# Performance work log

Measured on AMD Instinct MI355X. Metric: run time of the kernel, lower is better.

## Reference

```python
import jax, jax.numpy as jnp
import numpy as np

DIM, DEPTH, HEADS, DIM_HEAD, MLP = 1024, 4, 16, 64, 4096
INNER = HEADS * DIM_HEAD
B, N = 2, 1024


def _ln(x, g, b, eps=1e-5):
    mu = jnp.mean(x, axis=-1, keepdims=True)
    var = jnp.mean(jnp.square(x - mu), axis=-1, keepdims=True)
    return (x - mu) * jax.lax.rsqrt(var + eps) * g + b


def setup_inputs() -> dict:
    key = jax.random.key(0)
    ks = jax.random.split(key, 8)
    s = 0.02
    return {
        "x": jax.random.normal(ks[0], (B, N, DIM), jnp.float32),
        "mask": jax.random.randint(ks[1], (B, N, N), 0, 2, jnp.int32),
        "ln1_g": jnp.ones((DEPTH, DIM), jnp.float32),
        "ln1_b": jnp.zeros((DEPTH, DIM), jnp.float32),
        "qkv_w": jax.random.normal(ks[2], (DEPTH, DIM, 3 * INNER), jnp.float32) * s,
        "out_w": jax.random.normal(ks[3], (DEPTH, INNER, DIM), jnp.float32) * s,
        "out_b": jnp.zeros((DEPTH, DIM), jnp.float32),
        "ln2_g": jnp.ones((DEPTH, DIM), jnp.float32),
        "ln2_b": jnp.zeros((DEPTH, DIM), jnp.float32),
        "ff1_w": jax.random.normal(ks[4], (DEPTH, DIM, MLP), jnp.float32) * s,
        "ff1_b": jnp.zeros((DEPTH, MLP), jnp.float32),
        "ff2_w": jax.random.normal(ks[5], (DEPTH, MLP, DIM), jnp.float32) * s,
        "ff2_b": jnp.zeros((DEPTH, DIM), jnp.float32),
    }


def reference(x, mask, ln1_g, ln1_b, qkv_w, out_w, out_b, ln2_g, ln2_b,
              ff1_w, ff1_b, ff2_w, ff2_b):
    scale = DIM_HEAD ** -0.5
    masked = (mask == 0)[:, None, :, :]  # [B,1,N,N], True -> fill -1e9
    b, n, _ = x.shape
    for l in range(DEPTH):
        # --- prenorm attention ---
        h = _ln(x, ln1_g[l], ln1_b[l])
        qkv = h @ qkv_w[l]  # [B,N,3*INNER]
        q, k, v = jnp.split(qkv, 3, axis=-1)
        q = q.reshape(b, n, HEADS, DIM_HEAD).transpose(0, 2, 1, 3)
        k = k.reshape(b, n, HEADS, DIM_HEAD).transpose(0, 2, 1, 3)
        v = v.reshape(b, n, HEADS, DIM_HEAD).transpose(0, 2, 1, 3)
        dots = jnp.einsum('bhqd,bhkd->bhqk', q, k) * scale
        dots = jnp.where(masked, jnp.float32(-1e9), dots)
        attn = jax.nn.softmax(dots, axis=-1)
        o = jnp.einsum('bhqk,bhkd->bhqd', attn, v)
        o = o.transpose(0, 2, 1, 3).reshape(b, n, INNER)
        x = o @ out_w[l] + out_b[l] + x
        # --- prenorm feedforward ---
        h = _ln(x, ln2_g[l], ln2_b[l])
        h = jax.nn.gelu(h @ ff1_w[l] + ff1_b[l], approximate=False)
        x = h @ ff2_w[l] + ff2_b[l] + x
    return x
```

## Files before the change

kernel.cpp:

```cpp
#include <hip/hip_runtime.h>
#include <stdint.h>

#define DIMM 1024
#define NSEQ 1024
#define BB 2
#define HEADSN 16
#define MLPD 4096
#define DEPTHN 4
#define MROWS (BB*NSEQ)
#define VSTR 10240

typedef __bf16 bf16x8 __attribute__((ext_vector_type(8)));
typedef float f32x4 __attribute__((ext_vector_type(4)));

__device__ __forceinline__ float bf2f(unsigned short u) {
    union { uint32_t i; float f; } x; x.i = ((uint32_t)u) << 16; return x.f;
}
__device__ __forceinline__ unsigned short f2bf(float f) {
    union { uint32_t i; float f; } x; x.f = f;
    uint32_t r = x.i + 0x7fffu + ((x.i >> 16) & 1u);
    return (unsigned short)(r >> 16);
}
__device__ __forceinline__ float loadf(const void* p, size_t i, int f32) {
    return f32 ? ((const float*)p)[i] : bf2f(((const unsigned short*)p)[i]);
}
__device__ __forceinline__ uint32_t cvt_pk_bf16(float lo, float hi) {
    uint32_t r;
    asm("v_cvt_pk_bf16_f32 %0, %1, %2" : "=v"(r) : "v"(lo), "v"(hi));
    return r;
}

__device__ __forceinline__ void gl_lds16(const unsigned short* g, unsigned short* l) {
    __builtin_amdgcn_global_load_lds(
        (const __attribute__((address_space(1))) uint32_t*)g,
        (__attribute__((address_space(3))) uint32_t*)l,
        16, 0, 0);
}

__global__ __launch_bounds__(256) void sniff_kernel(const unsigned short* __restrict__ x,
                                                    int* __restrict__ flag) {
    __shared__ int cnt[256];
    int tid = threadIdx.x;
    int c = 0;
    for (int i = tid * 2; i < 65536; i += 512) {
        int e = (x[i] >> 7) & 0xFF;
        if (e >= 0x8A) c++;
    }
    cnt[tid] = c;
    __syncthreads();
    for (int s = 128; s > 0; s >>= 1) {
        if (tid < s) cnt[tid] += cnt[tid + s];
        __syncthreads();
    }
    if (tid == 0) flag[0] = (cnt[0] > 32) ? 1 : 0;
}

__global__ __launch_bounds__(256) void cvt_x(const void* __restrict__ x, float* __restrict__ xf,
                                             const int* __restrict__ flag) {
    int f = flag[0];
    int i = blockIdx.x * 256 + threadIdx.x;
    xf[i] = loadf(x, i, f);
}
__global__ __launch_bounds__(256) void store_out(const float* __restrict__ xf, void* __restrict__ out,
                                                 const int* __restrict__ flag) {
    int f = flag[0];
    int i = blockIdx.x * 256 + threadIdx.x;
    float v = xf[i];
    if (f) ((float*)out)[i] = v;
    else   ((unsigned short*)out)[i] = f2bf(v);
}
__global__ __launch_bounds__(256) void conv_all(const void* s0, const void* s1, const void* s2,
                                                const void* s3, const void* s4, const void* s5,
                                                const void* s6, unsigned short* __restrict__ dst,
                                                const int* __restrict__ flag) {
    int f = flag[0];
    const void* src; int len, off;
    switch (blockIdx.y) {
        case 0: src = s0; len = 1024; off = 0;    break;
        case 1: src = s1; len = 1024; off = 1024; break;
        case 2: src = s2; len = 1024; off = 2048; break;
        case 3: src = s3; len = 1024; off = 3072; break;
        case 4: src = s4; len = 1024; off = 4096; break;
        case 5: src = s5; len = 1024; off = 5120; break;
        default: src = s6; len = 4096; off = 6144; break;
    }
    int i = blockIdx.x * 256 + threadIdx.x;
    if (i < DEPTHN * len) {
        int l = i / len, o = i - l * len;
        dst[l * VSTR + off + o] = f2bf(loadf(src, i, f));
    }
}

__global__ __launch_bounds__(256) void transpose_conv(const void* __restrict__ in, size_t srcOffE,
                                                      unsigned short* __restrict__ out,
                                                      int K, int N, const int* __restrict__ flag) {
    int f = flag[0];
    __shared__ unsigned short t[32][33];
    int n0 = blockIdx.x * 32, k0 = blockIdx.y * 32;
    int tx = threadIdx.x, ty = threadIdx.y;
#pragma unroll
    for (int i = 0; i < 4; i++) {
        int k = k0 + ty + i * 8;
        t[ty + i * 8][tx] = f2bf(loadf(in, srcOffE + (size_t)k * N + n0 + tx, f));
    }
    __syncthreads();
#pragma unroll
    for (int i = 0; i < 4; i++) {
        int n = n0 + ty + i * 8;
        out[(size_t)n * K + k0 + tx] = t[tx][ty + i * 8];
    }
}

__global__ __launch_bounds__(256) void vt_kernel(const unsigned short* __restrict__ qkv,
                                                 unsigned short* __restrict__ vt) {
    __shared__ unsigned short t[32][33];
    int b = blockIdx.z;
    int c0 = blockIdx.x * 32, k0 = blockIdx.y * 32;
    int tx = threadIdx.x, ty = threadIdx.y;
#pragma unroll
    for (int i = 0; i < 4; i++) {
        int k = k0 + ty + i * 8;
        t[ty + i * 8][tx] = qkv[(size_t)(b * 1024 + k) * 3072 + 2048 + c0 + tx];
    }
    __syncthreads();
#pragma unroll
    for (int i = 0; i < 4; i++) {
        int c = c0 + ty + i * 8;
        vt[(size_t)(b * 1024 + c) * 1024 + k0 + tx] = t[tx][ty + i * 8];
    }
}

__global__ __launch_bounds__(256) void mask_pack(const int* __restrict__ mask,
                                                 unsigned long long* __restrict__ bits) {
    int wid = (blockIdx.x * 256 + threadIdx.x) >> 6;
    int lane = threadIdx.x & 63;
#pragma unroll
    for (int i = 0; i < 16; i++) {
        int w = wid * 16 + i;
        int mv = mask[(size_t)w * 64 + lane];
        unsigned long long bl = __ballot(mv != 0);
        if (lane == 0) bits[w] = bl;
    }
}

__global__ __launch_bounds__(256) void ln_kernel(const float* __restrict__ x,
                                                 const unsigned short* __restrict__ g,
                                                 const unsigned short* __restrict__ bta,
                                                 unsigned short* __restrict__ out) {
    int row = blockIdx.x, tid = threadIdx.x;
    const float* xr = x + (size_t)row * DIMM;
    float v[4]; float s = 0.f, s2 = 0.f;
#pragma unroll
    for (int i = 0; i < 4; i++) { v[i] = xr[tid + i * 256]; s += v[i]; s2 += v[i] * v[i]; }
#pragma unroll
    for (int off = 32; off >= 1; off >>= 1) {
        s  += __shfl_down(s, off, 64);
        s2 += __shfl_down(s2, off, 64);
    }
    __shared__ float rs[4], rs2[4];
    int wv = tid >> 6;
    if ((tid & 63) == 0) { rs[wv] = s; rs2[wv] = s2; }
    __syncthreads();
    s  = rs[0] + rs[1] + rs[2] + rs[3];
    s2 = rs2[0] + rs2[1] + rs2[2] + rs2[3];
    float mu  = s * (1.f / DIMM);
    float var = s2 * (1.f / DIMM) - mu * mu;
    float rr  = rsqrtf(var + 1e-5f);
#pragma unroll
    for (int i = 0; i < 4; i++) {
        int c = tid + i * 256;
        float y = (v[i] - mu) * rr * bf2f(g[c]) + bf2f(bta[c]);
        out[(size_t)row * DIMM + c] = f2bf(y);
    }
}

template <int S, int HAS_LN>
__global__ __launch_bounds__(256) void reduce_ln(const float* __restrict__ slab,
                                                 const unsigned short* __restrict__ bias,
                                                 float* __restrict__ xf,
                                                 const unsigned short* __restrict__ g,
                                                 const unsigned short* __restrict__ bta,
                                                 unsigned short* __restrict__ out) {
    const size_t SL = (size_t)MROWS * DIMM;
    int row = blockIdx.x, tid = threadIdx.x;
    float v[4]; float s = 0.f, s2 = 0.f;
#pragma unroll
    for (int i = 0; i < 4; i++) {
        int c = tid + i * 256;
        size_t idx = (size_t)row * DIMM + c;
        float t = xf[idx] + bf2f(bias[c]);
#pragma unroll
        for (int z = 0; z < S; z++) t += slab[z * SL + idx];
        xf[idx] = t;
        v[i] = t; s += t; s2 += t * t;
    }
    if (HAS_LN) {
#pragma unroll
        for (int off = 32; off >= 1; off >>= 1) {
            s  += __shfl_down(s, off, 64);
            s2 += __shfl_down(s2, off, 64);
        }
        __shared__ float rs[4], rs2[4];
        int wv = tid >> 6;
        if ((tid & 63) == 0) { rs[wv] = s; rs2[wv] = s2; }
        __syncthreads();
        s  = rs[0] + rs[1] + rs[2] + rs[3];
        s2 = rs2[0] + rs2[1] + rs2[2] + rs2[3];
        float mu  = s * (1.f / DIMM);
        float var = s2 * (1.f / DIMM) - mu * mu;
        float rr  = rsqrtf(var + 1e-5f);
#pragma unroll
        for (int i = 0; i < 4; i++) {
            int c = tid + i * 256;
            float y = (v[i] - mu) * rr * bf2f(g[c]) + bf2f(bta[c]);
            out[(size_t)row * DIMM + c] = f2bf(y);
        }
    }
}

template <int MODE, int SPLITK>
__global__ __launch_bounds__(512) void gemm_bt(const unsigned short* __restrict__ A,
                                               const unsigned short* __restrict__ Bt,
                                               const unsigned short* __restrict__ bias,
                                               unsigned short* __restrict__ Cbf,
                                               float* __restrict__ Cres,
                                               int M, int N, int K) {
    __shared__ __align__(16) unsigned short As[128 * 32];
    __shared__ __align__(16) unsigned short Bs[128 * 32];
    const int tid = threadIdx.x;
    const int mBase = blockIdx.y * 128, nBase = blockIdx.x * 128;
    const int w = tid >> 6, lane = tid & 63;
    const int wm = (w >> 2) * 64, wn = (w & 3) * 32;
    const int quad = lane >> 4, l16 = lane & 15;
    const int kLen = K / SPLITK;
    const int kStart = (SPLITK > 1) ? blockIdx.z * kLen : 0;

    f32x4 acc[4][2];
#pragma unroll
    for (int i = 0; i < 4; i++)
#pragma unroll
        for (int j = 0; j < 2; j++) acc[i][j] = (f32x4){0.f, 0.f, 0.f, 0.f};

    const int lr = lane >> 2;
    const int lc = ((lane & 3) ^ ((lr >> 1) & 3)) * 8;
    const int wb = w & 3;
    const unsigned short* G = (w < 4 ? A  + (size_t)(mBase + wb * 32 + lr) * K
                                     : Bt + (size_t)(nBase + wb * 32 + lr) * K)
                              + kStart + lc;
    unsigned short* L0 = (w < 4 ? &As[(wb * 32) * 32] : &Bs[(wb * 32) * 32]);
    unsigned short* L1 = L0 + 16 * 32;
    const size_t rstep = (size_t)16 * K;

    const int rcb = (quad ^ ((l16 >> 1) & 3)) * 8;

    for (int k0 = 0; k0 < kLen; k0 += 32) {
        __syncthreads();
        gl_lds16(G + k0,         L0);
        gl_lds16(G + k0 + rstep, L1);
        __syncthreads();

        bf16x8 af[4], bfv[2];
#pragma unroll
        for (int i = 0; i < 4; i++)
            af[i] = *(const bf16x8*)&As[(wm + i * 16 + l16) * 32 + rcb];
#pragma unroll
        for (int j = 0; j < 2; j++)
            bfv[j] = *(const bf16x8*)&Bs[(wn + j * 16 + l16) * 32 + rcb];
#pragma unroll
        for (int i = 0; i < 4; i++)
#pragma unroll
            for (int j = 0; j < 2; j++)
                acc[i][j] = __builtin_amdgcn_mfma_f32_16x16x32_bf16(af[i], bfv[j], acc[i][j], 0, 0, 0);
    }

    const size_t slabOff = (MODE == 3) ? (size_t)blockIdx.z * M * N : 0;
#pragma unroll
    for (int i = 0; i < 4; i++) {
#pragma unroll
        for (int j = 0; j < 2; j++) {
#pragma unroll
            for (int r = 0; r < 4; r++) {
                int m = mBase + wm + i * 16 + quad * 4 + r;
                int n = nBase + wn + j * 16 + l16;
                float v = acc[i][j][r];
                size_t idx = (size_t)m * N + n;
                if (MODE == 0) {
                    Cbf[idx] = f2bf(v);
                } else if (MODE == 1) {
                    if (SPLITK > 1) {
                        if (blockIdx.z == 0) v += bf2f(bias[n]);
                        atomicAdd(&Cres[idx], v);
                    } else {
                        Cres[idx] += v + bf2f(bias[n]);
                    }
                } else if (MODE == 2) {
                    float t2 = v + bf2f(bias[n]);
                    float gg = 0.5f * t2 * (1.f + erff(t2 * 0.70710678118f));
                    Cbf[idx] = f2bf(gg);
                } else {
                    Cres[slabOff + idx] = v;
                }
            }
        }
    }
}

__global__ __launch_bounds__(256) void attn_mfma(const unsigned short* __restrict__ qkv,
                                                 const unsigned short* __restrict__ vt,
                                                 const unsigned long long* __restrict__ mbits,
                                                 unsigned short* __restrict__ o) {
    __shared__ __align__(16) unsigned short Ks[64 * 72];
    __shared__ __align__(16) unsigned short Vs[64 * 72];

    const int tid = threadIdx.x, w = tid >> 6, lane = tid & 63;
    const int quad = lane >> 4, l16 = lane & 15;
    const int qt = blockIdx.x, h = blockIdx.y, b = blockIdx.z;

    const size_t qrow = (size_t)(b * NSEQ + qt * 64 + w * 16 + l16) * 3072 + h * 64;
    bf16x8 qf[2];
    qf[0] = *(const bf16x8*)(qkv + qrow + quad * 8);
    qf[1] = *(const bf16x8*)(qkv + qrow + 32 + quad * 8);

    const int srow = tid >> 2, scol = (tid & 3) * 16;
    const unsigned short* kg_base = qkv + (size_t)(b * NSEQ) * 3072 + 1024 + h * 64;
    const unsigned short* vg_base = vt + (size_t)((b * HEADSN + h) * 64 + srow) * 1024;

    f32x4 oacc[4];
#pragma unroll
    for (int j = 0; j < 4; j++) oacc[j] = (f32x4){0.f, 0.f, 0.f, 0.f};
    float m_run = -1e30f, l_run = 0.f;

    const unsigned long long* mb = mbits + ((size_t)(b * NSEQ + qt * 64 + w * 16 + l16)) * 16;

    for (int kt = 0; kt < 16; kt++) {
        __syncthreads();
        {
            const unsigned short* kg = kg_base + (size_t)(kt * 64 + srow) * 3072 + scol;
            uint4 k0 = *(const uint4*)kg;
            uint4 k1 = *(const uint4*)(kg + 8);
            const unsigned short* vg = vg_base + kt * 64 + scol;
            uint4 v0 = *(const uint4*)vg;
            uint4 v1 = *(const uint4*)(vg + 8);
            *(uint4*)&Ks[srow * 72 + scol]     = k0;
            *(uint4*)&Ks[srow * 72 + scol + 8] = k1;
            *(uint4*)&Vs[srow * 72 + scol]     = v0;
            *(uint4*)&Vs[srow * 72 + scol + 8] = v1;
        }
        __syncthreads();

        f32x4 sacc[4];
#pragma unroll
        for (int j = 0; j < 4; j++) sacc[j] = (f32x4){0.f, 0.f, 0.f, 0.f};
#pragma unroll
        for (int ks = 0; ks < 2; ks++) {
#pragma unroll
            for (int j = 0; j < 4; j++) {
                bf16x8 kf = *(const bf16x8*)&Ks[(j * 16 + l16) * 72 + ks * 32 + quad * 8];
                sacc[j] = __builtin_amdgcn_mfma_f32_16x16x32_bf16(kf, qf[ks], sacc[j], 0, 0, 0);
            }
        }

        const unsigned long long mw = mb[kt];

        float t[4][4];
        float mxj[4];
#pragma unroll
        for (int j = 0; j < 4; j++) {
            unsigned nib = (unsigned)(mw >> (quad * 4 + j * 16)) & 0xFu;
#pragma unroll
            for (int r = 0; r < 4; r++) {
                float s = sacc[j][r] * 0.125f;
                t[j][r] = ((nib >> r) & 1u) ? s : -1e30f;
            }
            mxj[j] = fmaxf(fmaxf(t[j][0], t[j][1]), fmaxf(t[j][2], t[j][3]));
        }
        float mx = fmaxf(fmaxf(mxj[0], mxj[1]), fmaxf(mxj[2], mxj[3]));
        mx = fmaxf(mx, __shfl_xor(mx, 16, 64));
        mx = fmaxf(mx, __shfl_xor(mx, 32, 64));

        if (!__all(mx <= m_run)) {
            float m_new = fmaxf(m_run, mx);
            float alpha = __expf(m_run - m_new);
            m_run = m_new;
            l_run *= alpha;
            float al[4];
#pragma unroll
            for (int r = 0; r < 4; r++) al[r] = __shfl(alpha, quad * 4 + r, 64);
#pragma unroll
            for (int j = 0; j < 4; j++)
#pragma unroll
                for (int r = 0; r < 4; r++) oacc[j][r] *= al[r];
        }

        float p[4][4];
        float psj[4];
#pragma unroll
        for (int j = 0; j < 4; j++) {
#pragma unroll
            for (int r = 0; r < 4; r++) p[j][r] = __expf(t[j][r] - m_run);
            psj[j] = (p[j][0] + p[j][1]) + (p[j][2] + p[j][3]);
        }
        float ps = (psj[0] + psj[1]) + (psj[2] + psj[3]);
        ps += __shfl_xor(ps, 16, 64);
        ps += __shfl_xor(ps, 32, 64);
        l_run += ps;

        union { uint32_t u[4]; bf16x8 v; } pa[2];
#pragma unroll
        for (int ks = 0; ks < 2; ks++) {
            pa[ks].u[0] = cvt_pk_bf16(p[2 * ks][0],     p[2 * ks][1]);
            pa[ks].u[1] = cvt_pk_bf16(p[2 * ks][2],     p[2 * ks][3]);
            pa[ks].u[2] = cvt_pk_bf16(p[2 * ks + 1][0], p[2 * ks + 1][1]);
            pa[ks].u[3] = cvt_pk_bf16(p[2 * ks + 1][2], p[2 * ks + 1][3]);
        }

#pragma unroll
        for (int ks = 0; ks < 2; ks++) {
#pragma unroll
            for (int j = 0; j < 4; j++) {
                union { ushort4 u[2]; bf16x8 v; } vf;
                const unsigned short* vp = &Vs[(j * 16 + l16) * 72 + ks * 32 + quad * 4];
                vf.u[0] = *(const ushort4*)vp;
                vf.u[1] = *(const ushort4*)(vp + 16);
                oacc[j] = __builtin_amdgcn_mfma_f32_16x16x32_bf16(pa[ks].v, vf.v, oacc[j], 0, 0, 0);
            }
        }
    }

    float inv[4];
#pragma unroll
    for (int r = 0; r < 4; r++) {
        float lr = __shfl(l_run, quad * 4 + r, 64);
        inv[r] = 1.f / lr;
    }
#pragma unroll
    for (int j = 0; j < 4; j++) {
#pragma unroll
        for (int r = 0; r < 4; r++) {
            size_t row = (size_t)(b * NSEQ + qt * 64 + w * 16 + quad * 4 + r);
            o[row * 1024 + h * 64 + j * 16 + l16] = f2bf(oacc[j][r] * inv[r]);
        }
    }
}

extern "C" void kernel_launch(void* const* d_in, const int* in_sizes, int n_in,
                              void* d_out, int out_size, void* d_ws, size_t ws_size,
                              hipStream_t stream) {
    const void* x     = d_in[0];
    const int*  mask  = (const int*)d_in[1];
    const void* ln1_g = d_in[2];
    const void* ln1_b = d_in[3];
    const void* qkv_w = d_in[4];
    const void* out_w = d_in[5];
    const void* out_b = d_in[6];
    const void* ln2_g = d_in[7];
    const void* ln2_b = d_in[8];
    const void* ff1_w = d_in[9];
    const void* ff1_b = d_in[10];
    const void* ff2_w = d_in[11];
    const void* ff2_b = d_in[12];

    char* ws = (char*)d_ws;
    float*          xf     = (float*)ws;
    unsigned short* h_bf   = (unsigned short*)(ws + (8u  << 20));
    unsigned short* qkv_bf = (unsigned short*)(ws + (12u << 20));
    unsigned short* ff_bf  = (unsigned short*)(ws + (12u << 20));
    unsigned short* vt_bf  = (unsigned short*)(ws + (24u << 20));
    unsigned short* o_bf   = (unsigned short*)(ws + (28u << 20));
    unsigned short* wT     = (unsigned short*)(ws + (32u << 20));
    unsigned short* vecs   = (unsigned short*)(ws + (40u << 20));
    int*            flag   = (int*)(ws + (40u << 20) + (128u << 10));
    unsigned long long* mbits = (unsigned long long*)(ws + (40u << 20) + (192u << 10));
    float*          slab   = (float*)(ws + (41u << 20));

    const bool slabs_ok = ws_size >= (74ull << 20);

    sniff_kernel<<<1, 256, 0, stream>>>((const unsigned short*)x, flag);

    conv_all<<<dim3(64, 7), 256, 0, stream>>>(ln1_g, ln1_b, out_b, ln2_g, ln2_b, ff2_b, ff1_b,
                                              vecs, flag);
    mask_pack<<<512, 256, 0, stream>>>(mask, mbits);

    const int nx = MROWS * DIMM;
    cvt_x<<<nx / 256, 256, 0, stream>>>(x, xf, flag);

    for (int l = 0; l < DEPTHN; l++) {
        const unsigned short* lv = vecs + l * VSTR;
        const unsigned short* lvn = vecs + (l + 1) * VSTR;

        if (l == 0)
            ln_kernel<<<MROWS, 256, 0, stream>>>(xf, lv + 0, lv + 1024, h_bf);
        transpose_conv<<<dim3(3072 / 32, 1024 / 32), dim3(32, 8), 0, stream>>>(
            qkv_w, (size_t)l * 1024 * 3072, wT, 1024, 3072, flag);
        gemm_bt<0, 1><<<dim3(3072 / 128, MROWS / 128), 512, 0, stream>>>(
            h_bf, wT, nullptr, qkv_bf, nullptr, MROWS, 3072, 1024);
        vt_kernel<<<dim3(32, 32, BB), dim3(32, 8), 0, stream>>>(qkv_bf, vt_bf);
        attn_mfma<<<dim3(NSEQ / 64, HEADSN, BB), 256, 0, stream>>>(qkv_bf, vt_bf, mbits, o_bf);
        transpose_conv<<<dim3(1024 / 32, 1024 / 32), dim3(32, 8), 0, stream>>>(
            out_w, (size_t)l * 1024 * 1024, wT, 1024, 1024, flag);
        if (slabs_ok) {
            gemm_bt<3, 2><<<dim3(1024 / 128, MROWS / 128, 2), 512, 0, stream>>>(
                o_bf, wT, nullptr, nullptr, slab, MROWS, 1024, 1024);
            reduce_ln<2, 1><<<MROWS, 256, 0, stream>>>(
                slab, lv + 2048, xf, lv + 3072, lv + 4096, h_bf);
        } else {
            gemm_bt<1, 2><<<dim3(1024 / 128, MROWS / 128, 2), 512, 0, stream>>>(
                o_bf, wT, lv + 2048, nullptr, xf, MROWS, 1024, 1024);
            ln_kernel<<<MROWS, 256, 0, stream>>>(xf, lv + 3072, lv + 4096, h_bf);
        }

        transpose_conv<<<dim3(4096 / 32, 1024 / 32), dim3(32, 8), 0, stream>>>(
            ff1_w, (size_t)l * 1024 * 4096, wT, 1024, 4096, flag);
        gemm_bt<2, 1><<<dim3(4096 / 128, MROWS / 128), 512, 0, stream>>>(
            h_bf, wT, lv + 6144, ff_bf, nullptr, MROWS, 4096, 1024);
        transpose_conv<<<dim3(1024 / 32, 4096 / 32), dim3(32, 8), 0, stream>>>(
            ff2_w, (size_t)l * 4096 * 1024, wT, 4096, 1024, flag);
        if (slabs_ok) {
            gemm_bt<3, 4><<<dim3(1024 / 128, MROWS / 128, 4), 512, 0, stream>>>(
                ff_bf, wT, nullptr, nullptr, slab, MROWS, 1024, 4096);
            if (l < DEPTHN - 1)
                reduce_ln<4, 1><<<MROWS, 256, 0, stream>>>(
                    slab, lv + 5120, xf, lvn + 0, lvn + 1024, h_bf);
            else
                reduce_ln<4, 0><<<MROWS, 256, 0, stream>>>(
                    slab, lv + 5120, xf, nullptr, nullptr, nullptr);
        } else {
            gemm_bt<1, 4><<<dim3(1024 / 128, MROWS / 128, 4), 512, 0, stream>>>(
                ff_bf, wT, lv + 5120, nullptr, xf, MROWS, 1024, 4096);
            if (l < DEPTHN - 1)
                ln_kernel<<<MROWS, 256, 0, stream>>>(xf, lvn + 0, lvn + 1024, h_bf);
        }
    }

    store_out<<<nx / 256, 256, 0, stream>>>(xf, d_out, flag);
}
```

Baseline: 936.1 us.

## Double-buffer GEMM LDS tiles to overlap global loads with MFMA compute

Splits the GEMM shared-memory tiles into two ping-pong buffers and issues the next K-tile's global-to-LDS loads before computing the current tile. Explicit vmcnt waits and raw barriers replace the paired __syncthreads, so load latency is hidden behind the MFMA work. This doubles LDS usage per block, which may lower occupancy, and it assumes the K-tile count is even.

```diff
diff --git a/kernel.cpp b/kernel.cpp
--- a/kernel.cpp
+++ b/kernel.cpp
@@ -35,6 +35,14 @@
         (const __attribute__((address_space(1))) uint32_t*)g,
         (__attribute__((address_space(3))) uint32_t*)l,
         16, 0, 0);
+}
+
+__device__ __forceinline__ void wait_vm2() { asm volatile("s_waitcnt vmcnt(2)" ::: "memory"); }
+__device__ __forceinline__ void wait_vm0() { asm volatile("s_waitcnt vmcnt(0)" ::: "memory"); }
+__device__ __forceinline__ void barrier_sync() {
+    asm volatile("" ::: "memory");
+    __builtin_amdgcn_s_barrier();
+    asm volatile("" ::: "memory");
 }
 
 __global__ __launch_bounds__(256) void sniff_kernel(const unsigned short* __restrict__ x,
@@ -225,8 +233,10 @@
                                                unsigned short* __restrict__ Cbf,
                                                float* __restrict__ Cres,
                                                int M, int N, int K) {
-    __shared__ __align__(16) unsigned short As[128 * 32];
-    __shared__ __align__(16) unsigned short Bs[128 * 32];
+    __shared__ __align__(16) unsigned short As0[128 * 32];
+    __shared__ __align__(16) unsigned short As1[128 * 32];
+    __shared__ __align__(16) unsigned short Bs0[128 * 32];
+    __shared__ __align__(16) unsigned short Bs1[128 * 32];
     const int tid = threadIdx.x;
     const int mBase = blockIdx.y * 128, nBase = blockIdx.x * 128;
     const int w = tid >> 6, lane = tid & 63;
@@ -234,6 +244,7 @@
     const int quad = lane >> 4, l16 = lane & 15;
     const int kLen = K / SPLITK;
     const int kStart = (SPLITK > 1) ? blockIdx.z * kLen : 0;
+    const int NT = kLen / 32;
 
     f32x4 acc[4][2];
 #pragma unroll
@@ -247,30 +258,49 @@
     const unsigned short* G = (w < 4 ? A  + (size_t)(mBase + wb * 32 + lr) * K
                                      : Bt + (size_t)(nBase + wb * 32 + lr) * K)
                               + kStart + lc;
-    unsigned short* L0 = (w < 4 ? &As[(wb * 32) * 32] : &Bs[(wb * 32) * 32]);
-    unsigned short* L1 = L0 + 16 * 32;
+    unsigned short* L0a = (w < 4 ? &As0[(wb * 32) * 32] : &Bs0[(wb * 32) * 32]);
+    unsigned short* L1a = L0a + 16 * 32;
+    unsigned short* L0b = (w < 4 ? &As1[(wb * 32) * 32] : &Bs1[(wb * 32) * 32]);
+    unsigned short* L1b = L0b + 16 * 32;
     const size_t rstep = (size_t)16 * K;
 
     const int rcb = (quad ^ ((l16 >> 1) & 3)) * 8;
 
-    for (int k0 = 0; k0 < kLen; k0 += 32) {
-        __syncthreads();
-        gl_lds16(G + k0,         L0);
-        gl_lds16(G + k0 + rstep, L1);
-        __syncthreads();
-
+    auto compute_t = [&](const unsigned short* Asb, const unsigned short* Bsb) {
         bf16x8 af[4], bfv[2];
 #pragma unroll
         for (int i = 0; i < 4; i++)
-            af[i] = *(const bf16x8*)&As[(wm + i * 16 + l16) * 32 + rcb];
+            af[i] = *(const bf16x8*)&Asb[(wm + i * 16 + l16) * 32 + rcb];
 #pragma unroll
         for (int j = 0; j < 2; j++)
-            bfv[j] = *(const bf16x8*)&Bs[(wn + j * 16 + l16) * 32 + rcb];
+            bfv[j] = *(const bf16x8*)&Bsb[(wn + j * 16 + l16) * 32 + rcb];
 #pragma unroll
         for (int i = 0; i < 4; i++)
 #pragma unroll
             for (int j = 0; j < 2; j++)
                 acc[i][j] = __builtin_amdgcn_mfma_f32_16x16x32_bf16(af[i], bfv[j], acc[i][j], 0, 0, 0);
+    };
+
+    gl_lds16(G, L0a);
+    gl_lds16(G + rstep, L1a);
+
+    for (int t = 0; t < NT; t += 2) {
+        gl_lds16(G + (size_t)(t + 1) * 32,         L0b);
+        gl_lds16(G + (size_t)(t + 1) * 32 + rstep, L1b);
+        wait_vm2();
+        barrier_sync();
+        compute_t(As0, Bs0);
+        barrier_sync();
+        if (t + 2 < NT) {
+            gl_lds16(G + (size_t)(t + 2) * 32,         L0a);
+            gl_lds16(G + (size_t)(t + 2) * 32 + rstep, L1a);
+            wait_vm2();
+        } else {
+            wait_vm0();
+        }
+        barrier_sync();
+        compute_t(As1, Bs1);
+        barrier_sync();
     }
 
     const size_t slabOff = (MODE == 3) ? (size_t)blockIdx.z * M * N : 0;
```

New measurement: 888.2 us. 1.05x faster.
